# Kernel optimization log

Measured on AMD Instinct MI355X. Metric: run time of the kernel, lower is better.

## Reference

```python
import math
import jax, jax.numpy as jnp
import numpy as np

FACTOR = 5


def setup_inputs() -> dict:
    key = jax.random.key(0)
    kq, kk, kv, ki = jax.random.split(key, 4)
    B, H, L, D = 4, 8, 2048, 64
    sample_k = min(FACTOR * math.ceil(math.log(L)), L)  # 40
    queries = jax.random.normal(kq, (B, H, L, D), dtype=jnp.float32)
    keys = jax.random.normal(kk, (B, H, L, D), dtype=jnp.float32)
    values = jax.random.normal(kv, (B, H, L, D), dtype=jnp.float32)
    index_sample = jax.random.randint(ki, (L, sample_k), 0, L, dtype=jnp.int64 if jax.config.jax_enable_x64 else jnp.int32)
    return {"queries": queries, "keys": keys, "values": values, "index_sample": index_sample}


def reference(queries, keys, values, index_sample):
    B, H, L_Q, D = queries.shape
    L_K = keys.shape[2]
    u = min(FACTOR * math.ceil(math.log(L_Q)), L_Q)  # n_top queries (= 40)
    scale = 1.0 / math.sqrt(D)

    # --- _prob_QK: sparsity measurement over randomly sampled keys ---
    # K_sample[b,h,q,s,:] = keys[b,h,index_sample[q,s],:]  -> [B,H,L_Q,S,D]
    K_sample = keys[:, :, index_sample, :]
    Q_K_sample = jnp.einsum('bhqd,bhqsd->bhqs', queries, K_sample)  # [B,H,L_Q,S]
    M = Q_K_sample.max(axis=-1) - Q_K_sample.sum(axis=-1) / L_K      # [B,H,L_Q]
    _, M_top = jax.lax.top_k(M, u)                                    # [B,H,u]

    Q_reduce = jnp.take_along_axis(queries, M_top[..., None], axis=2)  # [B,H,u,D]
    scores_top = jnp.einsum('bhud,bhkd->bhuk', Q_reduce, keys) * scale  # [B,H,u,L_K]

    # --- initial context: causal cumulative sum of V (mask_flag=True) ---
    context = jnp.cumsum(values, axis=2)  # [B,H,L_Q,D]

    # --- ProbMask: causal rows gathered at the selected query indices ---
    causal = jnp.triu(jnp.ones((L_Q, L_K), dtype=bool), 1)  # [L_Q,L_K]
    mask = causal[M_top]                                     # [B,H,u,L_K]
    scores_top = jnp.where(mask, -jnp.inf, scores_top)

    attn = jax.nn.softmax(scores_top, axis=-1)                       # [B,H,u,L_K]
    update = jnp.einsum('bhuk,bhkd->bhud', attn, values)             # [B,H,u,D]

    b_idx = jnp.arange(B)[:, None, None]
    h_idx = jnp.arange(H)[None, :, None]
    context = context.at[b_idx, h_idx, M_top].set(update.astype(context.dtype))
    return context
```

## Files before the change

### kernel.cpp

```cpp
#include <hip/hip_runtime.h>
#include <math.h>

#define BB 4
#define HH 8
#define LL 2048
#define DD 64
#define SK 40
#define BH (BB*HH)

__device__ __forceinline__ unsigned ordu(float v) {
    unsigned u = __float_as_uint(v);
    return (u & 0x80000000u) ? ~u : (u | 0x80000000u);
}

__global__ __launch_bounds__(256) void stage1_kernel(
        const float* __restrict__ Q, const float* __restrict__ K,
        const float* __restrict__ V, const int* __restrict__ IDX,
        float* __restrict__ M, float* __restrict__ csum) {
    int tid = threadIdx.x;
    if (blockIdx.x < 1024) {
        int x = blockIdx.x;
        int bhLo = x & 7;
        int r = x >> 3;
        int bhHi = r & 3;
        int chunk = r >> 2;
        int bh = bhHi * 8 + bhLo;
        int qbase = chunk * 64;
        int w = tid >> 6, lane = tid & 63;
        int qw = lane >> 2, c = lane & 3;
        int qi = w * 16 + qw;
        int qpos = qbase + qi;

        __shared__ int sidx[64 * SK];
        for (int i = tid; i < 64 * SK; i += 256) sidx[i] = IDX[(size_t)qbase * SK + i];

        const float4* Q4 = (const float4*)Q;
        const float4* K4 = (const float4*)K;
        float4 qreg[4];
        #pragma unroll
        for (int j = 0; j < 4; ++j)
            qreg[j] = Q4[((size_t)bh * LL + qpos) * 16 + j * 4 + c];
        __syncthreads();

        size_t kb4 = (size_t)bh * LL * 16;
        const int* myidx = sidx + qi * SK;

        int iA = myidx[0], iB = myidx[1];
        float4 A[4], B[4];
        #pragma unroll
        for (int j = 0; j < 4; ++j) {
            A[j] = K4[kb4 + (size_t)iA * 16 + j * 4 + c];
            B[j] = K4[kb4 + (size_t)iB * 16 + j * 4 + c];
        }
        int iC = myidx[2], iD = myidx[3];

        float mx = -INFINITY, sm = 0.f;
        for (int s = 0; s < SK; s += 2) {
            float4 Cr[4], Dr[4];
            if (s + 2 < SK) {
                #pragma unroll
                for (int j = 0; j < 4; ++j) {
                    Cr[j] = K4[kb4 + (size_t)iC * 16 + j * 4 + c];
                    Dr[j] = K4[kb4 + (size_t)iD * 16 + j * 4 + c];
                }
                if (s + 4 < SK) { iC = myidx[s + 4]; iD = myidx[s + 5]; }
            }
            float p0 = 0.f, p1 = 0.f;
            #pragma unroll
            for (int j = 0; j < 4; ++j) {
                p0 += A[j].x * qreg[j].x + A[j].y * qreg[j].y + A[j].z * qreg[j].z + A[j].w * qreg[j].w;
                p1 += B[j].x * qreg[j].x + B[j].y * qreg[j].y + B[j].z * qreg[j].z + B[j].w * qreg[j].w;
            }
            p0 += __shfl_xor(p0, 1, 64);
            p0 += __shfl_xor(p0, 2, 64);
            p1 += __shfl_xor(p1, 1, 64);
            p1 += __shfl_xor(p1, 2, 64);
            mx = fmaxf(mx, fmaxf(p0, p1));
            sm += p0 + p1;
            #pragma unroll
            for (int j = 0; j < 4; ++j) { A[j] = Cr[j]; B[j] = Dr[j]; }
        }
        if (c == 0) M[(size_t)bh * LL + qpos] = mx - sm * (1.0f / (float)LL);
    } else {
        int x = blockIdx.x - 1024;
        int bhLo = x & 7, r = x >> 3;
        int bhHi = r & 3, c = r >> 2;
        int bh = bhHi * 8 + bhLo;
        int d = tid & 63, sg = tid >> 6;
        size_t base = (size_t)bh * LL * DD;
        int row0 = c * 128 + sg * 32;
        float s = 0.f;
        for (int j = 0; j < 32; ++j) s += V[base + (size_t)(row0 + j) * DD + d];
        __shared__ float part[4][DD];
        part[sg][d] = s;
        __syncthreads();
        if (sg == 0)
            csum[((size_t)bh * 16 + c) * DD + d] = part[0][d] + part[1][d] + part[2][d] + part[3][d];
    }
}

__global__ __launch_bounds__(256) void stage2_kernel(
        const float* __restrict__ V, const float* __restrict__ csum,
        const float* __restrict__ M, float* __restrict__ out,
        int* __restrict__ topk) {
    int tid = threadIdx.x;
    if (blockIdx.x < 512) {
        int x = blockIdx.x;
        int bhLo = x & 7, r = x >> 3;
        int bhHi = r & 3, c = r >> 2;
        int bh = bhHi * 8 + bhLo;
        int d = tid & 63, sg = tid >> 6;
        size_t base = (size_t)bh * LL * DD;
        int row0 = c * 128 + sg * 32;
        float v[32];
        #pragma unroll
        for (int j = 0; j < 32; ++j) v[j] = V[base + (size_t)(row0 + j) * DD + d];
        float s = 0.f;
        #pragma unroll
        for (int j = 0; j < 32; ++j) s += v[j];
        __shared__ float part[4][DD];
        part[sg][d] = s;
        __syncthreads();
        float pre = 0.f;
        for (int cc = 0; cc < c; ++cc) pre += csum[((size_t)bh * 16 + cc) * DD + d];
        for (int ss = 0; ss < sg; ++ss) pre += part[ss][d];
        float acc = pre;
        #pragma unroll
        for (int j = 0; j < 32; ++j) {
            acc += v[j];
            out[base + (size_t)(row0 + j) * DD + d] = acc;
        }
    } else {
        int bh = blockIdx.x - 512;
        __shared__ unsigned hist[256];
        __shared__ unsigned bc_prefix, bc_need;
        __shared__ unsigned cnt_gt, cnt_eq;
        __shared__ int eqlist[128];
        __shared__ int sel[SK];

        unsigned v[8];
        #pragma unroll
        for (int j = 0; j < 8; ++j)
            v[j] = ordu(M[(size_t)bh * LL + tid + j * 256]);

        unsigned prefix = 0, need = SK;
        #pragma unroll
        for (int pass = 0; pass < 4; ++pass) {
            const int s = 24 - 8 * pass;
            const unsigned maskHigh = (pass == 0) ? 0u : (0xFFFFFFFFu << (s + 8));
            hist[tid] = 0;
            __syncthreads();
            #pragma unroll
            for (int j = 0; j < 8; ++j)
                if (((v[j] ^ prefix) & maskHigh) == 0)
                    atomicAdd(&hist[(v[j] >> s) & 0xFF], 1u);
            __syncthreads();
            unsigned above = 0;
            for (int b = tid + 1; b < 256; ++b) above += hist[b];
            if (above < need && above + hist[tid] >= need) {
                bc_prefix = prefix | ((unsigned)tid << s);
                bc_need = need - above;
            }
            __syncthreads();
            prefix = bc_prefix;
            need = bc_need;
            __syncthreads();
        }
        unsigned T = prefix;
        if (tid == 0) { cnt_gt = 0; cnt_eq = 0; }
        __syncthreads();
        #pragma unroll
        for (int j = 0; j < 8; ++j) {
            int idx = tid + j * 256;
            if (v[j] > T) { unsigned p = atomicAdd(&cnt_gt, 1u); sel[p] = idx; }
            else if (v[j] == T) { unsigned p = atomicAdd(&cnt_eq, 1u); if (p < 128) eqlist[p] = idx; }
        }
        __syncthreads();
        if (tid == 0) {
            int ne = (int)min(cnt_eq, 128u);
            unsigned base = cnt_gt;
            for (unsigned r2 = 0; r2 < need; ++r2) {
                int bj = 0, bv = 0x7FFFFFFF;
                for (int j = 0; j < ne; ++j)
                    if (eqlist[j] < bv) { bv = eqlist[j]; bj = j; }
                sel[base + r2] = bv;
                eqlist[bj] = 0x7FFFFFFF;
            }
        }
        __syncthreads();
        if (tid < SK) {
            int mine = sel[tid];
            int rank = 0;
            #pragma unroll
            for (int j = 0; j < SK; ++j) rank += (sel[j] > mine);
            topk[bh * SK + rank] = mine;
        }
    }
}

__global__ __launch_bounds__(256) void attn_kernel(
        const float* __restrict__ Q, const float* __restrict__ K,
        const float* __restrict__ V, const int* __restrict__ topk,
        float* __restrict__ out) {
    int x = blockIdx.x;
    int bh = x & 31;
    int u = x >> 5;
    int tid = threadIdx.x;

    int qpos = topk[bh * SK + u];
    int nk = qpos + 1;

    const float4* Q4 = (const float4*)Q;
    const float4* K4 = (const float4*)K;
    const float4* V4 = (const float4*)V;

    int w = tid >> 6, lane = tid & 63;
    int kw = lane >> 2, c = lane & 3;
    float4 qreg[4];
    #pragma unroll
    for (int j = 0; j < 4; ++j)
        qreg[j] = Q4[((size_t)bh * LL + qpos) * 16 + j * 4 + c];

    __shared__ float sc[LL];
    __shared__ float red[4], red2[4];
    __shared__ float opart[16][16][4];

    size_t kb4 = (size_t)bh * LL * 16;
    int rounds = (nk + 63) >> 6;
    int key0 = w * 16 + kw;
    float4 A[4];
    if (key0 < nk) {
        #pragma unroll
        for (int j = 0; j < 4; ++j) A[j] = K4[kb4 + (size_t)key0 * 16 + j * 4 + c];
    }
    for (int rr = 0; rr < rounds; ++rr) {
        int key = rr * 64 + key0;
        int keyn = key + 64;
        float4 B[4];
        if (rr + 1 < rounds && keyn < nk) {
            #pragma unroll
            for (int j = 0; j < 4; ++j) B[j] = K4[kb4 + (size_t)keyn * 16 + j * 4 + c];
        }
        if (key < nk) {
            float p = 0.f;
            #pragma unroll
            for (int j = 0; j < 4; ++j)
                p += A[j].x * qreg[j].x + A[j].y * qreg[j].y + A[j].z * qreg[j].z + A[j].w * qreg[j].w;
            p += __shfl_xor(p, 1, 64);
            p += __shfl_xor(p, 2, 64);
            if (c == 0) sc[key] = p * 0.125f;
        }
        #pragma unroll
        for (int j = 0; j < 4; ++j) A[j] = B[j];
    }
    __syncthreads();

    float m = -INFINITY;
    for (int j = tid; j < nk; j += 256) m = fmaxf(m, sc[j]);
    #pragma unroll
    for (int off = 32; off > 0; off >>= 1) m = fmaxf(m, __shfl_xor(m, off, 64));
    if (lane == 0) red[w] = m;
    __syncthreads();
    m = fmaxf(fmaxf(red[0], red[1]), fmaxf(red[2], red[3]));

    float ls = 0.f;
    for (int j = tid; j < nk; j += 256) {
        float e = expf(sc[j] - m);
        sc[j] = e;
        ls += e;
    }
    #pragma unroll
    for (int off = 32; off > 0; off >>= 1) ls += __shfl_xor(ls, off, 64);
    if (lane == 0) red2[w] = ls;
    __syncthreads();
    float linv = 1.0f / (red2[0] + red2[1] + red2[2] + red2[3]);

    int col4 = tid & 15, kg = tid >> 4;
    float ax = 0.f, ay = 0.f, az = 0.f, aw = 0.f;
    size_t vb4 = (size_t)bh * LL * 16;
    float4 Va = make_float4(0.f, 0.f, 0.f, 0.f);
    float4 Vb = make_float4(0.f, 0.f, 0.f, 0.f);
    if (kg < nk)      Va = V4[vb4 + (size_t)kg * 16 + col4];
    if (kg + 16 < nk) Vb = V4[vb4 + (size_t)(kg + 16) * 16 + col4];
    for (int j = kg; j < nk; j += 16) {
        float4 Vc = make_float4(0.f, 0.f, 0.f, 0.f);
        if (j + 32 < nk) Vc = V4[vb4 + (size_t)(j + 32) * 16 + col4];
        float sj = sc[j];
        ax += sj * Va.x; ay += sj * Va.y; az += sj * Va.z; aw += sj * Va.w;
        Va = Vb; Vb = Vc;
    }
    opart[kg][col4][0] = ax;
    opart[kg][col4][1] = ay;
    opart[kg][col4][2] = az;
    opart[kg][col4][3] = aw;
    __syncthreads();
    if (tid < DD) {
        int c4 = tid >> 2, cp = tid & 3;
        float s = 0.f;
        #pragma unroll
        for (int kg2 = 0; kg2 < 16; ++kg2) s += opart[kg2][c4][cp];
        out[((size_t)bh * LL + qpos) * DD + tid] = s * linv;
    }
}

extern "C" void kernel_launch(void* const* d_in, const int* in_sizes, int n_in,
                              void* d_out, int out_size, void* d_ws, size_t ws_size,
                              hipStream_t stream) {
    const float* Q   = (const float*)d_in[0];
    const float* K   = (const float*)d_in[1];
    const float* V   = (const float*)d_in[2];
    const int*   IDX = (const int*)d_in[3];
    float* out = (float*)d_out;

    char* ws = (char*)d_ws;
    float* M    = (float*)ws;  ws += (size_t)BH * LL * sizeof(float);
    int*   topk = (int*)ws;    ws += ((size_t)BH * SK * sizeof(int) + 255) & ~255ull;
    float* csum = (float*)ws;

    stage1_kernel<<<1536, 256, 0, stream>>>(Q, K, V, IDX, M, csum);
    stage2_kernel<<<544, 256, 0, stream>>>(V, csum, M, out, topk);
    attn_kernel<<<BH * SK, 256, 0, stream>>>(Q, K, V, topk, out);
}
```

Measured before the change: 169.0 us.

## Batch four top-k queries per attention block and split sampled keys across lanes

The attention kernel now handles four selected queries per block, sorted descending so the first has the longest causal range. Each K and V row is loaded once and reused for all four queries, with masked entries set to -inf. Stage 1 splits each query's 40 sampled keys across two 4-lane groups and merges max and sum with a shuffle, doubling the block count for more parallelism. The trade-off is more registers for four query vectors and extra work on the longest key range for the shorter queries in each group.

```diff
diff --git a/kernel.cpp b/kernel.cpp
--- a/kernel.cpp
+++ b/kernel.cpp
@@ -7,6 +7,7 @@
 #define DD 64
 #define SK 40
 #define BH (BB*HH)
+#define NG 10
 
 __device__ __forceinline__ unsigned ordu(float v) {
     unsigned u = __float_as_uint(v);
@@ -18,21 +19,23 @@
         const float* __restrict__ V, const int* __restrict__ IDX,
         float* __restrict__ M, float* __restrict__ csum) {
     int tid = threadIdx.x;
-    if (blockIdx.x < 1024) {
+    if (blockIdx.x < 2048) {
         int x = blockIdx.x;
         int bhLo = x & 7;
         int r = x >> 3;
         int bhHi = r & 3;
         int chunk = r >> 2;
         int bh = bhHi * 8 + bhLo;
-        int qbase = chunk * 64;
+        int qbase = chunk * 32;
         int w = tid >> 6, lane = tid & 63;
-        int qw = lane >> 2, c = lane & 3;
-        int qi = w * 16 + qw;
+        int c = lane & 3;
+        int h = (lane >> 2) & 1;
+        int qw = lane >> 3;
+        int qi = w * 8 + qw;
         int qpos = qbase + qi;
 
-        __shared__ int sidx[64 * SK];
-        for (int i = tid; i < 64 * SK; i += 256) sidx[i] = IDX[(size_t)qbase * SK + i];
+        __shared__ int sidx[32 * SK];
+        for (int i = tid; i < 32 * SK; i += 256) sidx[i] = IDX[(size_t)qbase * SK + i];
 
         const float4* Q4 = (const float4*)Q;
         const float4* K4 = (const float4*)K;
@@ -43,27 +46,27 @@
         __syncthreads();
 
         size_t kb4 = (size_t)bh * LL * 16;
-        const int* myidx = sidx + qi * SK;
-
-        int iA = myidx[0], iB = myidx[1];
+        const int* my = sidx + qi * SK + h * 20;
+
+        int iA = my[0], iB = my[1];
         float4 A[4], B[4];
         #pragma unroll
         for (int j = 0; j < 4; ++j) {
             A[j] = K4[kb4 + (size_t)iA * 16 + j * 4 + c];
             B[j] = K4[kb4 + (size_t)iB * 16 + j * 4 + c];
         }
-        int iC = myidx[2], iD = myidx[3];
+        int iC = my[2], iD = my[3];
 
         float mx = -INFINITY, sm = 0.f;
-        for (int s = 0; s < SK; s += 2) {
+        for (int s = 0; s < 20; s += 2) {
             float4 Cr[4], Dr[4];
-            if (s + 2 < SK) {
+            if (s + 2 < 20) {
                 #pragma unroll
                 for (int j = 0; j < 4; ++j) {
                     Cr[j] = K4[kb4 + (size_t)iC * 16 + j * 4 + c];
                     Dr[j] = K4[kb4 + (size_t)iD * 16 + j * 4 + c];
                 }
-                if (s + 4 < SK) { iC = myidx[s + 4]; iD = myidx[s + 5]; }
+                if (s + 4 < 20) { iC = my[s + 4]; iD = my[s + 5]; }
             }
             float p0 = 0.f, p1 = 0.f;
             #pragma unroll
@@ -80,9 +83,11 @@
             #pragma unroll
             for (int j = 0; j < 4; ++j) { A[j] = Cr[j]; B[j] = Dr[j]; }
         }
-        if (c == 0) M[(size_t)bh * LL + qpos] = mx - sm * (1.0f / (float)LL);
+        mx = fmaxf(mx, __shfl_xor(mx, 4, 64));
+        sm += __shfl_xor(sm, 4, 64);
+        if ((lane & 7) == 0) M[(size_t)bh * LL + qpos] = mx - sm * (1.0f / (float)LL);
     } else {
-        int x = blockIdx.x - 1024;
+        int x = blockIdx.x - 2048;
         int bhLo = x & 7, r = x >> 3;
         int bhHi = r & 3, c = r >> 2;
         int bh = bhHi * 8 + bhLo;
@@ -204,102 +209,131 @@
         float* __restrict__ out) {
     int x = blockIdx.x;
     int bh = x & 31;
-    int u = x >> 5;
+    int g = x >> 5;
     int tid = threadIdx.x;
 
-    int qpos = topk[bh * SK + u];
-    int nk = qpos + 1;
+    int qp[4];
+    #pragma unroll
+    for (int i = 0; i < 4; ++i) qp[i] = topk[bh * SK + g * 4 + i];
+    int nk = qp[0] + 1;
 
     const float4* Q4 = (const float4*)Q;
     const float4* K4 = (const float4*)K;
     const float4* V4 = (const float4*)V;
 
     int w = tid >> 6, lane = tid & 63;
-    int kw = lane >> 2, c = lane & 3;
-    float4 qreg[4];
-    #pragma unroll
-    for (int j = 0; j < 4; ++j)
-        qreg[j] = Q4[((size_t)bh * LL + qpos) * 16 + j * 4 + c];
-
-    __shared__ float sc[LL];
-    __shared__ float red[4], red2[4];
+    int c = lane & 3, kw = lane >> 2;
+
+    float4 qreg[4][4];
+    #pragma unroll
+    for (int i = 0; i < 4; ++i)
+        #pragma unroll
+        for (int j = 0; j < 4; ++j)
+            qreg[i][j] = Q4[((size_t)bh * LL + qp[i]) * 16 + j * 4 + c];
+
+    __shared__ float sc[4][LL];
+    __shared__ float red[4][4], red2[4][4];
     __shared__ float opart[16][16][4];
 
     size_t kb4 = (size_t)bh * LL * 16;
     int rounds = (nk + 63) >> 6;
-    int key0 = w * 16 + kw;
-    float4 A[4];
-    if (key0 < nk) {
-        #pragma unroll
-        for (int j = 0; j < 4; ++j) A[j] = K4[kb4 + (size_t)key0 * 16 + j * 4 + c];
-    }
     for (int rr = 0; rr < rounds; ++rr) {
-        int key = rr * 64 + key0;
-        int keyn = key + 64;
-        float4 B[4];
-        if (rr + 1 < rounds && keyn < nk) {
-            #pragma unroll
-            for (int j = 0; j < 4; ++j) B[j] = K4[kb4 + (size_t)keyn * 16 + j * 4 + c];
-        }
+        int key = rr * 64 + w * 16 + kw;
         if (key < nk) {
-            float p = 0.f;
-            #pragma unroll
-            for (int j = 0; j < 4; ++j)
-                p += A[j].x * qreg[j].x + A[j].y * qreg[j].y + A[j].z * qreg[j].z + A[j].w * qreg[j].w;
-            p += __shfl_xor(p, 1, 64);
-            p += __shfl_xor(p, 2, 64);
-            if (c == 0) sc[key] = p * 0.125f;
-        }
-        #pragma unroll
-        for (int j = 0; j < 4; ++j) A[j] = B[j];
+            float4 A[4];
+            #pragma unroll
+            for (int j = 0; j < 4; ++j) A[j] = K4[kb4 + (size_t)key * 16 + j * 4 + c];
+            float p0 = 0.f, p1 = 0.f, p2 = 0.f, p3 = 0.f;
+            #pragma unroll
+            for (int j = 0; j < 4; ++j) {
+                p0 += A[j].x * qreg[0][j].x + A[j].y * qreg[0][j].y + A[j].z * qreg[0][j].z + A[j].w * qreg[0][j].w;
+                p1 += A[j].x * qreg[1][j].x + A[j].y * qreg[1][j].y + A[j].z * qreg[1][j].z + A[j].w * qreg[1][j].w;
+                p2 += A[j].x * qreg[2][j].x + A[j].y * qreg[2][j].y + A[j].z * qreg[2][j].z + A[j].w * qreg[2][j].w;
+                p3 += A[j].x * qreg[3][j].x + A[j].y * qreg[3][j].y + A[j].z * qreg[3][j].z + A[j].w * qreg[3][j].w;
+            }
+            p0 += __shfl_xor(p0, 1, 64); p0 += __shfl_xor(p0, 2, 64);
+            p1 += __shfl_xor(p1, 1, 64); p1 += __shfl_xor(p1, 2, 64);
+            p2 += __shfl_xor(p2, 1, 64); p2 += __shfl_xor(p2, 2, 64);
+            p3 += __shfl_xor(p3, 1, 64); p3 += __shfl_xor(p3, 2, 64);
+            if (c == 0) {
+                sc[0][key] = (key <= qp[0]) ? p0 * 0.125f : -INFINITY;
+                sc[1][key] = (key <= qp[1]) ? p1 * 0.125f : -INFINITY;
+                sc[2][key] = (key <= qp[2]) ? p2 * 0.125f : -INFINITY;
+                sc[3][key] = (key <= qp[3]) ? p3 * 0.125f : -INFINITY;
+            }
+        }
     }
     __syncthreads();
 
-    float m = -INFINITY;
-    for (int j = tid; j < nk; j += 256) m = fmaxf(m, sc[j]);
-    #pragma unroll
-    for (int off = 32; off > 0; off >>= 1) m = fmaxf(m, __shfl_xor(m, off, 64));
-    if (lane == 0) red[w] = m;
+    float m[4] = {-INFINITY, -INFINITY, -INFINITY, -INFINITY};
+    for (int j = tid; j < nk; j += 256) {
+        #pragma unroll
+        for (int i = 0; i < 4; ++i) m[i] = fmaxf(m[i], sc[i][j]);
+    }
+    #pragma unroll
+    for (int i = 0; i < 4; ++i) {
+        float mv = m[i];
+        #pragma unroll
+        for (int off = 32; off > 0; off >>= 1) mv = fmaxf(mv, __shfl_xor(mv, off, 64));
+        if (lane == 0) red[w][i] = mv;
+        m[i] = mv;
+    }
     __syncthreads();
-    m = fmaxf(fmaxf(red[0], red[1]), fmaxf(red[2], red[3]));
-
-    float ls = 0.f;
+    #pragma unroll
+    for (int i = 0; i < 4; ++i)
+        m[i] = fmaxf(fmaxf(red[0][i], red[1][i]), fmaxf(red[2][i], red[3][i]));
+
+    float l[4] = {0.f, 0.f, 0.f, 0.f};
     for (int j = tid; j < nk; j += 256) {
-        float e = expf(sc[j] - m);
-        sc[j] = e;
-        ls += e;
-    }
-    #pragma unroll
-    for (int off = 32; off > 0; off >>= 1) ls += __shfl_xor(ls, off, 64);
-    if (lane == 0) red2[w] = ls;
+        #pragma unroll
+        for (int i = 0; i < 4; ++i) {
+            float e = expf(sc[i][j] - m[i]);
+            sc[i][j] = e;
+            l[i] += e;
+        }
+    }
+    #pragma unroll
+    for (int i = 0; i < 4; ++i) {
+        float lv = l[i];
+        #pragma unroll
+        for (int off = 32; off > 0; off >>= 1) lv += __shfl_xor(lv, off, 64);
+        if (lane == 0) red2[w][i] = lv;
+    }
     __syncthreads();
-    float linv = 1.0f / (red2[0] + red2[1] + red2[2] + red2[3]);
+    float linv[4];
+    #pragma unroll
+    for (int i = 0; i < 4; ++i)
+        linv[i] = 1.0f / (red2[0][i] + red2[1][i] + red2[2][i] + red2[3][i]);
 
     int col4 = tid & 15, kg = tid >> 4;
-    float ax = 0.f, ay = 0.f, az = 0.f, aw = 0.f;
+    float4 acc[4];
+    #pragma unroll
+    for (int i = 0; i < 4; ++i) acc[i] = make_float4(0.f, 0.f, 0.f, 0.f);
     size_t vb4 = (size_t)bh * LL * 16;
-    float4 Va = make_float4(0.f, 0.f, 0.f, 0.f);
-    float4 Vb = make_float4(0.f, 0.f, 0.f, 0.f);
-    if (kg < nk)      Va = V4[vb4 + (size_t)kg * 16 + col4];
-    if (kg + 16 < nk) Vb = V4[vb4 + (size_t)(kg + 16) * 16 + col4];
     for (int j = kg; j < nk; j += 16) {
-        float4 Vc = make_float4(0.f, 0.f, 0.f, 0.f);
-        if (j + 32 < nk) Vc = V4[vb4 + (size_t)(j + 32) * 16 + col4];
-        float sj = sc[j];
-        ax += sj * Va.x; ay += sj * Va.y; az += sj * Va.z; aw += sj * Va.w;
-        Va = Vb; Vb = Vc;
-    }
-    opart[kg][col4][0] = ax;
-    opart[kg][col4][1] = ay;
-    opart[kg][col4][2] = az;
-    opart[kg][col4][3] = aw;
-    __syncthreads();
-    if (tid < DD) {
-        int c4 = tid >> 2, cp = tid & 3;
-        float s = 0.f;
-        #pragma unroll
-        for (int kg2 = 0; kg2 < 16; ++kg2) s += opart[kg2][c4][cp];
-        out[((size_t)bh * LL + qpos) * DD + tid] = s * linv;
+        float4 vv = V4[vb4 + (size_t)j * 16 + col4];
+        #pragma unroll
+        for (int i = 0; i < 4; ++i) {
+            float sj = sc[i][j];
+            acc[i].x += sj * vv.x; acc[i].y += sj * vv.y;
+            acc[i].z += sj * vv.z; acc[i].w += sj * vv.w;
+        }
+    }
+    #pragma unroll
+    for (int i = 0; i < 4; ++i) {
+        opart[kg][col4][0] = acc[i].x;
+        opart[kg][col4][1] = acc[i].y;
+        opart[kg][col4][2] = acc[i].z;
+        opart[kg][col4][3] = acc[i].w;
+        __syncthreads();
+        if (tid < DD) {
+            int c4 = tid >> 2, cp = tid & 3;
+            float s = 0.f;
+            #pragma unroll
+            for (int kg2 = 0; kg2 < 16; ++kg2) s += opart[kg2][c4][cp];
+            out[((size_t)bh * LL + qp[i]) * DD + tid] = s * linv[i];
+        }
+        __syncthreads();
     }
 }
 
@@ -317,7 +351,7 @@
     int*   topk = (int*)ws;    ws += ((size_t)BH * SK * sizeof(int) + 255) & ~255ull;
     float* csum = (float*)ws;
 
-    stage1_kernel<<<1536, 256, 0, stream>>>(Q, K, V, IDX, M, csum);
+    stage1_kernel<<<2560, 256, 0, stream>>>(Q, K, V, IDX, M, csum);
     stage2_kernel<<<544, 256, 0, stream>>>(V, csum, M, out, topk);
-    attn_kernel<<<BH * SK, 256, 0, stream>>>(Q, K, V, topk, out);
-}
+    attn_kernel<<<BH * NG, 256, 0, stream>>>(Q, K, V, topk, out);
+}
```

Result: slower. 178.7 us (+5.8%).
